# Kernel tuning notes

Hardware: AMD Instinct MI355X
Metric: run time of the kernel (lower is better)

The kernel has to match this reference:

```python
import jax, jax.numpy as jnp
import numpy as np

B, S, E, H = 2, 2048, 1024, 16
DH = E // H
SCALE = 1.0 / float(np.sqrt(E))  # note: original scales by 1/sqrt(hidden_dim), not head_dim


def _icl_mask(s):
    # triu(diagonal=0) is masked (-inf): only strictly-past positions visible,
    # except (0,0) which is explicitly unmasked so row 0 attends to itself.
    m = jnp.triu(jnp.ones((s, s), dtype=bool), k=0)
    return m.at[0, 0].set(False)


def setup_inputs() -> dict:
    key = jax.random.key(0)
    ks = jax.random.split(key, 7)
    mk = lambda k, shp: jax.random.normal(k, shp, dtype=jnp.float32)
    return {
        "q": mk(ks[0], (B, S, E)),
        "k": mk(ks[1], (B, S, E)),
        "v": mk(ks[2], (B, S, E)),
        "Wq": mk(ks[3], (E, E)) * 0.02,
        "Wk": mk(ks[4], (E, E)) * 0.02,
        "Wv": mk(ks[5], (E, E)) * 0.02,
        "Wo": mk(ks[6], (E, E)) * 0.02,
    }


def reference(q, k, v, Wq, Wk, Wv, Wo):
    b, s, e = q.shape
    h, dh = H, e // H
    # projections (nn.Linear: x @ W.T), split heads -> [b, h, s, dh]
    qh = (q @ Wq.T).reshape(b, s, h, dh).transpose(0, 2, 1, 3)
    kh = (k @ Wk.T).reshape(b, s, h, dh).transpose(0, 2, 1, 3)
    vh = (v @ Wv.T).reshape(b, s, h, dh).transpose(0, 2, 1, 3)
    scores = jnp.einsum("bhsd,bhtd->bhst", qh, kh) * SCALE  # [b,h,s,s]
    scores = jnp.where(_icl_mask(s), -jnp.inf, scores)
    probs = jax.nn.softmax(scores, axis=-1)
    out = jnp.einsum("bhst,bhtd->bhsd", probs, vh)
    out = out.transpose(0, 2, 1, 3).reshape(b, s, e)
    return out @ Wo.T
```

## Files before the change

kernel.cpp:

```cpp
#include <hip/hip_runtime.h>
#include <hip/hip_bf16.h>

typedef unsigned short u16;
typedef unsigned int u32;
typedef __bf16 bf16x8 __attribute__((ext_vector_type(8)));
typedef float float4_ __attribute__((ext_vector_type(4)));

#define B_ 2
#define S_ 2048
#define E_ 1024
#define H_ 16
#define DH_ 64
#define M_ (B_*S_)
#define SCALE_ 0.03125f
#define LOG2E_ 1.4426950408889634f

__device__ __forceinline__ u16 f2bf(float f) {
    unsigned int x = __float_as_uint(f);
    x += 0x7fffu + ((x >> 16) & 1u);
    return (u16)(x >> 16);
}

template <typename T> struct raw8;
template <> struct raw8<float> { float4_ lo, hi; };
template <> struct raw8<u16>   { bf16x8 v; };

__device__ __forceinline__ raw8<float> ldr8(const float* p) {
    raw8<float> r; const float4_* q = (const float4_*)p; r.lo = q[0]; r.hi = q[1]; return r;
}
__device__ __forceinline__ raw8<u16> ldr8(const u16* p) {
    raw8<u16> r; r.v = *(const bf16x8*)p; return r;
}
__device__ __forceinline__ bf16x8 cvt8(const raw8<u16>& r) { return r.v; }
__device__ __forceinline__ bf16x8 cvt8(const raw8<float>& r) {
    union { bf16x8 v; __hip_bfloat162 h[4]; } u;
    u.h[0] = __float22bfloat162_rn(float2{r.lo[0], r.lo[1]});
    u.h[1] = __float22bfloat162_rn(float2{r.lo[2], r.lo[3]});
    u.h[2] = __float22bfloat162_rn(float2{r.hi[0], r.hi[1]});
    u.h[3] = __float22bfloat162_rn(float2{r.hi[2], r.hi[3]});
    return u.v;
}
__device__ __forceinline__ bf16x8 ld8(const u16* p) { return *(const bf16x8*)p; }

__device__ __forceinline__ void async16(u16* lds, const u16* g) {
    __builtin_amdgcn_global_load_lds(
        (const __attribute__((address_space(1))) u32*)g,
        (__attribute__((address_space(3))) u32*)lds, 16, 0, 0);
}

__global__ __launch_bounds__(256)
void convw_kernel(const float* __restrict__ Wq, const float* __restrict__ Wk,
                  const float* __restrict__ Wv, const float* __restrict__ Wo,
                  u16* __restrict__ Wqb, u16* __restrict__ Wkb,
                  u16* __restrict__ Wvb, u16* __restrict__ Wob) {
    const int which = blockIdx.y;
    const float* src = which == 0 ? Wq : which == 1 ? Wk : which == 2 ? Wv : Wo;
    u16* dst        = which == 0 ? Wqb : which == 1 ? Wkb : which == 2 ? Wvb : Wob;
    size_t off = ((size_t)blockIdx.x * 256 + threadIdx.x) * 8;
    *(bf16x8*)&dst[off] = cvt8(ldr8(&src[off]));
}

__global__ __launch_bounds__(256)
void proj_kernel(const float* __restrict__ q, const float* __restrict__ k, const float* __restrict__ v,
                 const u16* __restrict__ Wqb, const u16* __restrict__ Wkb, const u16* __restrict__ Wvb,
                 u16* __restrict__ Qh, u16* __restrict__ Kh, u16* __restrict__ Vt) {
    const int z = blockIdx.z;
    const float* A = (z == 0) ? q : (z == 1) ? k : v;
    const u16* Wb  = (z == 0) ? Wqb : (z == 1) ? Wkb : Wvb;
    u16* C         = (z == 0) ? Qh : (z == 1) ? Kh : Vt;
    const float cscale = (z == 0) ? SCALE_ : 1.0f;
    const int transV = (z == 2);
    const int bm = blockIdx.x * 128, bn = blockIdx.y * 128;

    __shared__ u16 As[128 * 32];
    __shared__ u16 Bs[128 * 32];

    const int tid  = threadIdx.x;
    const int lane = tid & 63;
    const int w    = tid >> 6;
    const int wr   = (w >> 1) * 64, wc = (w & 1) * 64;
    const int m16  = lane & 15, quad = lane >> 4, q4 = quad * 4;
    const int row0 = tid >> 2, kc0 = (tid & 3) * 8, row1 = row0 + 64;
    const int c1   = tid + 256;

    u16* bs_d0 = (u16*)((char*)Bs + (size_t)tid * 16);
    u16* bs_d1 = (u16*)((char*)Bs + (size_t)c1 * 16);
    const u16* wg0 = &Wb[(size_t)(bn + (tid >> 2)) * 1024 + (tid & 3) * 8];
    const u16* wg1 = &Wb[(size_t)(bn + (c1 >> 2)) * 1024 + (c1 & 3) * 8];

    float4_ acc[4][4];
#pragma unroll
    for (int i = 0; i < 4; i++)
#pragma unroll
        for (int j = 0; j < 4; j++) acc[i][j] = (float4_){0.f, 0.f, 0.f, 0.f};

    raw8<float> pa0 = ldr8(&A[(size_t)(bm + row0) * 1024 + kc0]);
    raw8<float> pa1 = ldr8(&A[(size_t)(bm + row1) * 1024 + kc0]);

    for (int k0 = 0; k0 < 1024; k0 += 32) {
        __syncthreads();
        async16(bs_d0, wg0 + k0);
        async16(bs_d1, wg1 + k0);
        *(bf16x8*)&As[row0 * 32 + kc0] = cvt8(pa0);
        *(bf16x8*)&As[row1 * 32 + kc0] = cvt8(pa1);
        __syncthreads();
        if (k0 + 32 < 1024) {
            pa0 = ldr8(&A[(size_t)(bm + row0) * 1024 + k0 + 32 + kc0]);
            pa1 = ldr8(&A[(size_t)(bm + row1) * 1024 + k0 + 32 + kc0]);
        }
        bf16x8 af[4], bfr[4];
#pragma unroll
        for (int rt = 0; rt < 4; rt++)
            af[rt] = *(const bf16x8*)&As[(wr + rt * 16 + m16) * 32 + quad * 8];
#pragma unroll
        for (int ct = 0; ct < 4; ct++)
            bfr[ct] = *(const bf16x8*)&Bs[(wc + ct * 16 + m16) * 32 + quad * 8];
#pragma unroll
        for (int rt = 0; rt < 4; rt++)
#pragma unroll
            for (int ct = 0; ct < 4; ct++)
                acc[rt][ct] = __builtin_amdgcn_mfma_f32_16x16x32_bf16(af[rt], bfr[ct], acc[rt][ct], 0, 0, 0);
    }

#pragma unroll
    for (int rt = 0; rt < 4; rt++)
#pragma unroll
        for (int ct = 0; ct < 4; ct++)
#pragma unroll
            for (int r = 0; r < 4; r++) {
                int row = bm + wr + rt * 16 + q4 + r;
                int col = bn + wc + ct * 16 + m16;
                u16 val = f2bf(acc[rt][ct][r] * cscale);
                if (!transV) {
                    C[(size_t)row * 1024 + col] = val;
                } else {
                    int bb = row >> 11, s = row & 2047;
                    C[((size_t)(bb * 1024 + col)) * 2048 + s] = val;
                }
            }
}

__global__ __launch_bounds__(256)
void out_kernel(const u16* __restrict__ AO, const u16* __restrict__ Wob, float* __restrict__ C) {
    const int bm = blockIdx.x * 128, bn = blockIdx.y * 64;

    __shared__ u16 As[128 * 32];
    __shared__ u16 Bs[64 * 32];

    const int tid  = threadIdx.x;
    const int lane = tid & 63;
    const int w    = tid >> 6;
    const int m16  = lane & 15, quad = lane >> 4, q4 = quad * 4;
    const int c1   = tid + 256;

    u16* as_d0 = (u16*)((char*)As + (size_t)tid * 16);
    u16* as_d1 = (u16*)((char*)As + (size_t)c1 * 16);
    u16* bs_d  = (u16*)((char*)Bs + (size_t)tid * 16);
    const u16* ag0 = &AO[(size_t)(bm + (tid >> 2)) * 1024 + (tid & 3) * 8];
    const u16* ag1 = &AO[(size_t)(bm + (c1 >> 2)) * 1024 + (c1 & 3) * 8];
    const u16* bg  = &Wob[(size_t)(bn + (tid >> 2)) * 1024 + (tid & 3) * 8];

    float4_ acc[2][4];
#pragma unroll
    for (int i = 0; i < 2; i++)
#pragma unroll
        for (int j = 0; j < 4; j++) acc[i][j] = (float4_){0.f, 0.f, 0.f, 0.f};

    for (int k0 = 0; k0 < 1024; k0 += 32) {
        __syncthreads();
        async16(as_d0, ag0 + k0);
        async16(as_d1, ag1 + k0);
        async16(bs_d,  bg  + k0);
        __syncthreads();

        bf16x8 af[2], bfr[4];
#pragma unroll
        for (int rt = 0; rt < 2; rt++)
            af[rt] = *(const bf16x8*)&As[(w * 32 + rt * 16 + m16) * 32 + quad * 8];
#pragma unroll
        for (int ct = 0; ct < 4; ct++)
            bfr[ct] = *(const bf16x8*)&Bs[(ct * 16 + m16) * 32 + quad * 8];
#pragma unroll
        for (int rt = 0; rt < 2; rt++)
#pragma unroll
            for (int ct = 0; ct < 4; ct++)
                acc[rt][ct] = __builtin_amdgcn_mfma_f32_16x16x32_bf16(af[rt], bfr[ct], acc[rt][ct], 0, 0, 0);
    }

#pragma unroll
    for (int rt = 0; rt < 2; rt++)
#pragma unroll
        for (int ct = 0; ct < 4; ct++)
#pragma unroll
            for (int r = 0; r < 4; r++) {
                int row = bm + w * 32 + rt * 16 + q4 + r;
                int col = bn + ct * 16 + m16;
                C[(size_t)row * 1024 + col] = acc[rt][ct][r];
            }
}

__device__ __forceinline__ int sw64(int row, int col) {
    return row * 64 + ((((col >> 3) ^ (row & 7)) << 3) | (col & 7));
}

__global__ __launch_bounds__(256)
void attn_kernel(const u16* __restrict__ Qh, const u16* __restrict__ Kh,
                 const u16* __restrict__ Vt, u16* __restrict__ O) {
    const int h    = blockIdx.x;
    const int pair = blockIdx.y;
    const int tqA  = pair;
    const int tqB  = 31 - pair;
    const int b    = blockIdx.z;
    const int tid  = threadIdx.x;
    const int lane = tid & 63;
    const int w    = tid >> 6;
    const int m16  = lane & 15;
    const int quad = lane >> 4;
    const int q4   = quad * 4;

    __shared__ u16 Ks[2][64 * 64];
    __shared__ u16 Vs[2][64 * 64];
    __shared__ u16 PsA[64 * 64];
    __shared__ u16 PsB[64 * 64];

    const int srow0 = tid >> 3;
    const int skc0  = (tid & 7) * 8;
    const int sblk0 = ((skc0 >> 3) ^ (srow0 & 7)) << 3;
    const int srow1 = srow0 + 32;
    const int sblk1 = ((skc0 >> 3) ^ (srow1 & 7)) << 3;

    const size_t kbase = ((size_t)(b * S_)) * E_ + h * DH_;
    const size_t vbase = ((size_t)(b * 1024 + h * DH_)) * 2048;

    bf16x8 qfA[2], qfB[2];
    {
        const u16* qa = Qh + ((size_t)(b * S_ + tqA * 64 + w * 16 + m16)) * E_ + h * DH_;
        const u16* qb = Qh + ((size_t)(b * S_ + tqB * 64 + w * 16 + m16)) * E_ + h * DH_;
        qfA[0] = ld8(qa + quad * 8);  qfA[1] = ld8(qa + 32 + quad * 8);
        qfB[0] = ld8(qb + quad * 8);  qfB[1] = ld8(qb + 32 + quad * 8);
    }

    float lA[4] = {0.f, 0.f, 0.f, 0.f}, lB[4] = {0.f, 0.f, 0.f, 0.f};
    float4_ oA[4], oB[4];
#pragma unroll
    for (int dt = 0; dt < 4; dt++) { oA[dt] = (float4_){0.f,0.f,0.f,0.f}; oB[dt] = (float4_){0.f,0.f,0.f,0.f}; }

    *(bf16x8*)&Ks[0][srow0 * 64 + sblk0] = ld8(&Kh[kbase + (size_t)srow0 * E_ + skc0]);
    *(bf16x8*)&Ks[0][srow1 * 64 + sblk1] = ld8(&Kh[kbase + (size_t)srow1 * E_ + skc0]);
    *(bf16x8*)&Vs[0][srow0 * 64 + sblk0] = ld8(&Vt[vbase + (size_t)srow0 * 2048 + skc0]);
    *(bf16x8*)&Vs[0][srow1 * 64 + sblk1] = ld8(&Vt[vbase + (size_t)srow1 * 2048 + skc0]);
    __syncthreads();

    for (int t = 0; t <= tqB; t++) {
        const int cur = t & 1;

        bf16x8 kr0, kr1, vr0, vr1;
        const bool havepf = (t < tqB);
        if (havepf) {
            const size_t ko = kbase + (size_t)((t + 1) * 64) * E_;
            kr0 = ld8(&Kh[ko + (size_t)srow0 * E_ + skc0]);
            kr1 = ld8(&Kh[ko + (size_t)srow1 * E_ + skc0]);
            vr0 = ld8(&Vt[vbase + (size_t)srow0 * 2048 + (t + 1) * 64 + skc0]);
            vr1 = ld8(&Vt[vbase + (size_t)srow1 * 2048 + (t + 1) * 64 + skc0]);
        }

        auto process = [&](const bf16x8* qf, float* l_part, float4_* o_acc,
                           u16* Ps, int tqX) {
            const u16* Kc = &Ks[cur][0];
            const u16* Vc = &Vs[cur][0];
            float4_ sc[4];
#pragma unroll
            for (int ct = 0; ct < 4; ct++) sc[ct] = (float4_){0.f,0.f,0.f,0.f};
#pragma unroll
            for (int ks = 0; ks < 2; ks++)
#pragma unroll
                for (int ct = 0; ct < 4; ct++) {
                    bf16x8 kf = *(const bf16x8*)&Kc[sw64(ct * 16 + m16, ks * 32 + quad * 8)];
                    sc[ct] = __builtin_amdgcn_mfma_f32_16x16x32_bf16(qf[ks], kf, sc[ct], 0, 0, 0);
                }

            float p[4][4];
            if (t != tqX) {
#pragma unroll
                for (int ct = 0; ct < 4; ct++)
#pragma unroll
                    for (int r = 0; r < 4; r++) {
                        float pp = exp2f(sc[ct][r] * LOG2E_);
                        p[ct][r] = pp;
                        l_part[r] += pp;
                    }
            } else {
#pragma unroll
                for (int ct = 0; ct < 4; ct++)
#pragma unroll
                    for (int r = 0; r < 4; r++) {
                        int i_loc = w * 16 + q4 + r;
                        int j_loc = ct * 16 + m16;
                        bool allow = (j_loc < i_loc) || (tqX == 0 && i_loc == 0 && j_loc == 0);
                        float pp = allow ? exp2f(sc[ct][r] * LOG2E_) : 0.f;
                        p[ct][r] = pp;
                        l_part[r] += pp;
                    }
            }

#pragma unroll
            for (int ct = 0; ct < 4; ct++)
#pragma unroll
                for (int r = 0; r < 4; r++)
                    Ps[sw64(w * 16 + q4 + r, ct * 16 + m16)] = f2bf(p[ct][r]);

#pragma unroll
            for (int ks = 0; ks < 2; ks++) {
                bf16x8 pf = *(const bf16x8*)&Ps[sw64(w * 16 + m16, ks * 32 + quad * 8)];
#pragma unroll
                for (int dt = 0; dt < 4; dt++) {
                    bf16x8 vf = *(const bf16x8*)&Vc[sw64(dt * 16 + m16, ks * 32 + quad * 8)];
                    o_acc[dt] = __builtin_amdgcn_mfma_f32_16x16x32_bf16(pf, vf, o_acc[dt], 0, 0, 0);
                }
            }
        };

        process(qfB, lB, oB, PsB, tqB);
        if (t <= tqA) process(qfA, lA, oA, PsA, tqA);

        if (havepf) {
            const int nxt = cur ^ 1;
            *(bf16x8*)&Ks[nxt][srow0 * 64 + sblk0] = kr0;
            *(bf16x8*)&Ks[nxt][srow1 * 64 + sblk1] = kr1;
            *(bf16x8*)&Vs[nxt][srow0 * 64 + sblk0] = vr0;
            *(bf16x8*)&Vs[nxt][srow1 * 64 + sblk1] = vr1;
        }
        __syncthreads();
    }

    auto wrout = [&](const float4_* o_acc, const float* l_part, int tqX) {
        const size_t obase = ((size_t)(b * S_ + tqX * 64)) * E_ + h * DH_;
#pragma unroll
        for (int r = 0; r < 4; r++) {
            float l = l_part[r];
#pragma unroll
            for (int msk = 1; msk <= 8; msk <<= 1) l += __shfl_xor(l, msk);
            float inv_l = 1.0f / l;
            int row = w * 16 + q4 + r;
#pragma unroll
            for (int dt = 0; dt < 4; dt++) {
                int col = dt * 16 + m16;
                O[obase + (size_t)row * E_ + col] = f2bf(o_acc[dt][r] * inv_l);
            }
        }
    };
    wrout(oA, lA, tqA);
    wrout(oB, lB, tqB);
}

extern "C" void kernel_launch(void* const* d_in, const int* in_sizes, int n_in,
                              void* d_out, int out_size, void* d_ws, size_t ws_size,
                              hipStream_t stream) {
    const float* q  = (const float*)d_in[0];
    const float* k  = (const float*)d_in[1];
    const float* v  = (const float*)d_in[2];
    const float* Wq = (const float*)d_in[3];
    const float* Wk = (const float*)d_in[4];
    const float* Wv = (const float*)d_in[5];
    const float* Wo = (const float*)d_in[6];

    u16* ws  = (u16*)d_ws;
    u16* Qh  = ws;
    u16* Kh  = ws + (size_t)M_ * E_;
    u16* Vt  = ws + 2 * (size_t)M_ * E_;
    u16* AO  = ws + 3 * (size_t)M_ * E_;
    u16* Wqb = AO;
    u16* Wkb = AO + (size_t)E_ * E_;
    u16* Wvb = AO + 2 * (size_t)E_ * E_;
    u16* Wob = ws + 4 * (size_t)M_ * E_;

    dim3 blk(256);
    convw_kernel<<<dim3(512, 4), blk, 0, stream>>>(Wq, Wk, Wv, Wo, Wqb, Wkb, Wvb, Wob);
    proj_kernel<<<dim3(32, 8, 3), blk, 0, stream>>>(q, k, v, Wqb, Wkb, Wvb, Qh, Kh, Vt);
    attn_kernel<<<dim3(16, 16, 2), blk, 0, stream>>>(Qh, Kh, Vt, AO);
    out_kernel<<<dim3(32, 16), blk, 0, stream>>>(AO, Wob, (float*)d_out);
}
```

Before: 220.1 us.

## Double-buffer LDS tiles and XOR-swizzle layout in projection and output GEMMs

Both GEMM kernels now hold two LDS buffers per operand. The next K-tile's async global-to-LDS copy is issued before the MFMAs on the current tile, which removes one of the two barriers per iteration and overlaps memory with compute. The LDS layout also uses an XOR swizzle on 16-byte chunks to cut bank conflicts on the fragment reads. For the async copies, the swizzle is applied by permuting the global source addresses. This doubles LDS use per block, which may lower occupancy.

```diff
diff --git a/kernel.cpp b/kernel.cpp
--- a/kernel.cpp
+++ b/kernel.cpp
@@ -46,6 +46,10 @@
     __builtin_amdgcn_global_load_lds(
         (const __attribute__((address_space(1))) u32*)g,
         (__attribute__((address_space(3))) u32*)lds, 16, 0, 0);
+}
+
+__device__ __forceinline__ int swz32(int row, int col) {
+    return row * 32 + ((((col >> 3) ^ (row & 3)) << 3) | (col & 7));
 }
 
 __global__ __launch_bounds__(256)
@@ -72,8 +76,8 @@
     const int transV = (z == 2);
     const int bm = blockIdx.x * 128, bn = blockIdx.y * 128;
 
-    __shared__ u16 As[128 * 32];
-    __shared__ u16 Bs[128 * 32];
+    __shared__ u16 As[2][128 * 32];
+    __shared__ u16 Bs[2][128 * 32];
 
     const int tid  = threadIdx.x;
     const int lane = tid & 63;
@@ -82,11 +86,10 @@
     const int m16  = lane & 15, quad = lane >> 4, q4 = quad * 4;
     const int row0 = tid >> 2, kc0 = (tid & 3) * 8, row1 = row0 + 64;
     const int c1   = tid + 256;
-
-    u16* bs_d0 = (u16*)((char*)Bs + (size_t)tid * 16);
-    u16* bs_d1 = (u16*)((char*)Bs + (size_t)c1 * 16);
-    const u16* wg0 = &Wb[(size_t)(bn + (tid >> 2)) * 1024 + (tid & 3) * 8];
-    const u16* wg1 = &Wb[(size_t)(bn + (c1 >> 2)) * 1024 + (c1 & 3) * 8];
+    const int r1   = c1 >> 2;
+
+    const u16* wg0 = &Wb[(size_t)(bn + row0) * 1024 + (size_t)(((tid & 3) ^ (row0 & 3)) * 8)];
+    const u16* wg1 = &Wb[(size_t)(bn + r1)   * 1024 + (size_t)(((c1 & 3) ^ (r1 & 3)) * 8)];
 
     float4_ acc[4][4];
 #pragma unroll
@@ -97,29 +100,44 @@
     raw8<float> pa0 = ldr8(&A[(size_t)(bm + row0) * 1024 + kc0]);
     raw8<float> pa1 = ldr8(&A[(size_t)(bm + row1) * 1024 + kc0]);
 
-    for (int k0 = 0; k0 < 1024; k0 += 32) {
-        __syncthreads();
-        async16(bs_d0, wg0 + k0);
-        async16(bs_d1, wg1 + k0);
-        *(bf16x8*)&As[row0 * 32 + kc0] = cvt8(pa0);
-        *(bf16x8*)&As[row1 * 32 + kc0] = cvt8(pa1);
-        __syncthreads();
-        if (k0 + 32 < 1024) {
-            pa0 = ldr8(&A[(size_t)(bm + row0) * 1024 + k0 + 32 + kc0]);
-            pa1 = ldr8(&A[(size_t)(bm + row1) * 1024 + k0 + 32 + kc0]);
+    async16((u16*)((char*)Bs[0] + (size_t)tid * 16), wg0);
+    async16((u16*)((char*)Bs[0] + (size_t)c1 * 16), wg1);
+    *(bf16x8*)&As[0][swz32(row0, kc0)] = cvt8(pa0);
+    *(bf16x8*)&As[0][swz32(row1, kc0)] = cvt8(pa1);
+    pa0 = ldr8(&A[(size_t)(bm + row0) * 1024 + 32 + kc0]);
+    pa1 = ldr8(&A[(size_t)(bm + row1) * 1024 + 32 + kc0]);
+    __syncthreads();
+
+    auto step = [&](int t, const u16* Asc, const u16* Bsc, u16* Asn, u16* Bsn) {
+        if (t < 31) {
+            async16((u16*)((char*)Bsn + (size_t)tid * 16), wg0 + (t + 1) * 32);
+            async16((u16*)((char*)Bsn + (size_t)c1 * 16), wg1 + (t + 1) * 32);
+            *(bf16x8*)&Asn[swz32(row0, kc0)] = cvt8(pa0);
+            *(bf16x8*)&Asn[swz32(row1, kc0)] = cvt8(pa1);
+            if (t < 30) {
+                pa0 = ldr8(&A[(size_t)(bm + row0) * 1024 + (t + 2) * 32 + kc0]);
+                pa1 = ldr8(&A[(size_t)(bm + row1) * 1024 + (t + 2) * 32 + kc0]);
+            }
         }
+        __builtin_amdgcn_sched_barrier(0);
         bf16x8 af[4], bfr[4];
 #pragma unroll
         for (int rt = 0; rt < 4; rt++)
-            af[rt] = *(const bf16x8*)&As[(wr + rt * 16 + m16) * 32 + quad * 8];
+            af[rt] = *(const bf16x8*)&Asc[swz32(wr + rt * 16 + m16, quad * 8)];
 #pragma unroll
         for (int ct = 0; ct < 4; ct++)
-            bfr[ct] = *(const bf16x8*)&Bs[(wc + ct * 16 + m16) * 32 + quad * 8];
+            bfr[ct] = *(const bf16x8*)&Bsc[swz32(wc + ct * 16 + m16, quad * 8)];
 #pragma unroll
         for (int rt = 0; rt < 4; rt++)
 #pragma unroll
             for (int ct = 0; ct < 4; ct++)
                 acc[rt][ct] = __builtin_amdgcn_mfma_f32_16x16x32_bf16(af[rt], bfr[ct], acc[rt][ct], 0, 0, 0);
+        if (t < 31) __syncthreads();
+    };
+
+    for (int t = 0; t < 32; t += 2) {
+        step(t,     As[0], Bs[0], As[1], Bs[1]);
+        step(t + 1, As[1], Bs[1], As[0], Bs[0]);
     }
 
 #pragma unroll
@@ -144,8 +162,8 @@
 void out_kernel(const u16* __restrict__ AO, const u16* __restrict__ Wob, float* __restrict__ C) {
     const int bm = blockIdx.x * 128, bn = blockIdx.y * 64;
 
-    __shared__ u16 As[128 * 32];
-    __shared__ u16 Bs[64 * 32];
+    __shared__ u16 As[2][128 * 32];
+    __shared__ u16 Bs[2][64 * 32];
 
     const int tid  = threadIdx.x;
     const int lane = tid & 63;
@@ -153,12 +171,10 @@
     const int m16  = lane & 15, quad = lane >> 4, q4 = quad * 4;
     const int c1   = tid + 256;
 
-    u16* as_d0 = (u16*)((char*)As + (size_t)tid * 16);
-    u16* as_d1 = (u16*)((char*)As + (size_t)c1 * 16);
-    u16* bs_d  = (u16*)((char*)Bs + (size_t)tid * 16);
-    const u16* ag0 = &AO[(size_t)(bm + (tid >> 2)) * 1024 + (tid & 3) * 8];
-    const u16* ag1 = &AO[(size_t)(bm + (c1 >> 2)) * 1024 + (c1 & 3) * 8];
-    const u16* bg  = &Wob[(size_t)(bn + (tid >> 2)) * 1024 + (tid & 3) * 8];
+    const int swc = (((tid & 3) ^ ((tid >> 2) & 3)) * 8);
+    const u16* ag0 = &AO[(size_t)(bm + (tid >> 2)) * 1024 + swc];
+    const u16* ag1 = &AO[(size_t)(bm + (c1 >> 2)) * 1024 + swc];
+    const u16* bg  = &Wob[(size_t)(bn + (tid >> 2)) * 1024 + swc];
 
     float4_ acc[2][4];
 #pragma unroll
@@ -166,25 +182,36 @@
 #pragma unroll
         for (int j = 0; j < 4; j++) acc[i][j] = (float4_){0.f, 0.f, 0.f, 0.f};
 
-    for (int k0 = 0; k0 < 1024; k0 += 32) {
-        __syncthreads();
-        async16(as_d0, ag0 + k0);
-        async16(as_d1, ag1 + k0);
-        async16(bs_d,  bg  + k0);
-        __syncthreads();
-
+    async16((u16*)((char*)As[0] + (size_t)tid * 16), ag0);
+    async16((u16*)((char*)As[0] + (size_t)c1 * 16), ag1);
+    async16((u16*)((char*)Bs[0] + (size_t)tid * 16), bg);
+    __syncthreads();
+
+    auto step = [&](int t, const u16* Asc, const u16* Bsc, u16* Asn, u16* Bsn) {
+        if (t < 31) {
+            async16((u16*)((char*)Asn + (size_t)tid * 16), ag0 + (t + 1) * 32);
+            async16((u16*)((char*)Asn + (size_t)c1 * 16), ag1 + (t + 1) * 32);
+            async16((u16*)((char*)Bsn + (size_t)tid * 16), bg + (t + 1) * 32);
+        }
+        __builtin_amdgcn_sched_barrier(0);
         bf16x8 af[2], bfr[4];
 #pragma unroll
         for (int rt = 0; rt < 2; rt++)
-            af[rt] = *(const bf16x8*)&As[(w * 32 + rt * 16 + m16) * 32 + quad * 8];
+            af[rt] = *(const bf16x8*)&Asc[swz32(w * 32 + rt * 16 + m16, quad * 8)];
 #pragma unroll
         for (int ct = 0; ct < 4; ct++)
-            bfr[ct] = *(const bf16x8*)&Bs[(ct * 16 + m16) * 32 + quad * 8];
+            bfr[ct] = *(const bf16x8*)&Bsc[swz32(ct * 16 + m16, quad * 8)];
 #pragma unroll
         for (int rt = 0; rt < 2; rt++)
 #pragma unroll
             for (int ct = 0; ct < 4; ct++)
                 acc[rt][ct] = __builtin_amdgcn_mfma_f32_16x16x32_bf16(af[rt], bfr[ct], acc[rt][ct], 0, 0, 0);
+        if (t < 31) __syncthreads();
+    };
+
+    for (int t = 0; t < 32; t += 2) {
+        step(t,     As[0], Bs[0], As[1], Bs[1]);
+        step(t + 1, As[1], Bs[1], As[0], Bs[0]);
     }
 
 #pragma unroll
```

Result: slower. 226.4 us (+2.9%).
